# Kernel optimization log

Measured on AMD Instinct MI355X. Metric: run time of the kernel, lower is better.

The kernel has to match this reference:

```python
import jax, jax.numpy as jnp
import numpy as np

L, D, V, BS, H, HD, DL = 12, 768, 50257, 1024, 12, 64, 256
B, T = 2, 1024
EPS = 1e-5


def _ln(x, w, b):
    m = jnp.mean(x, axis=-1, keepdims=True)
    v = jnp.mean((x - m) ** 2, axis=-1, keepdims=True)
    return (x - m) * jax.lax.rsqrt(v + EPS) * w + b


def _rope_tables(t_len):
    inv_freq = 1.0 / (10000.0 ** (jnp.arange(0, HD, 2, dtype=jnp.float32) / HD))
    t = jnp.arange(t_len, dtype=jnp.float32)
    freqs = jnp.outer(t, inv_freq)  # [T, HD/2]
    return jnp.cos(freqs), jnp.sin(freqs)


def _apply_rope(x, cos, sin):
    # x: [B, H, T, HD]; cos/sin: [T, HD/2]
    c = jnp.concatenate([cos, cos], axis=-1)[None, None]
    s = jnp.concatenate([sin, sin], axis=-1)[None, None]
    x1, x2 = jnp.split(x, 2, axis=-1)
    rot = jnp.concatenate([-x2, x1], axis=-1)
    return x * c + rot * s


def setup_inputs() -> dict:
    key = jax.random.key(0)
    ks = jax.random.split(key, 16)
    std = 0.02
    n = lambda k, shape: jax.random.normal(k, shape, dtype=jnp.float32) * std
    return {
        'idx': jax.random.randint(ks[0], (B, T), 0, V),
        'wte': n(ks[1], (V, D)),
        'wpe': n(ks[2], (BS, D)),
        'ln1_w': jnp.ones((L, D)), 'ln1_b': jnp.zeros((L, D)),
        'wq_w': n(ks[3], (L, D, H * HD)), 'wq_b': jnp.zeros((L, H * HD)),
        'kva_w': n(ks[4], (L, D, DL)), 'kva_b': jnp.zeros((L, DL)),
        'kvb_w': n(ks[5], (L, DL, 2 * H * HD)), 'kvb_b': jnp.zeros((L, 2 * H * HD)),
        'out_w': n(ks[6], (L, H * HD, D)), 'out_b': jnp.zeros((L, D)),
        'ln2_w': jnp.ones((L, D)), 'ln2_b': jnp.zeros((L, D)),
        'fc_w': n(ks[7], (L, D, 4 * D)), 'fc_b': jnp.zeros((L, 4 * D)),
        'proj_w': n(ks[8], (L, 4 * D, D)), 'proj_b': jnp.zeros((L, D)),
        'lnf_w': jnp.ones((D,)), 'lnf_b': jnp.zeros((D,)),
    }


def _forward(idx, wte, wpe, ln1_w, ln1_b, wq_w, wq_b, kva_w, kva_b, kvb_w, kvb_b,
             out_w, out_b, ln2_w, ln2_b, fc_w, fc_b, proj_w, proj_b, lnf_w, lnf_b):
    b, t = idx.shape
    x = wte[idx] + wpe[:t][None]  # [B,T,D]
    cos, sin = _rope_tables(t)
    scale = 1.0 / np.sqrt(HD)
    causal = jnp.tril(jnp.ones((t, t), dtype=bool))
    for l in range(L):
        h = _ln(x, ln1_w[l], ln1_b[l])
        q = (h @ wq_w[l] + wq_b[l]).reshape(b, t, H, HD).transpose(0, 2, 1, 3)
        kv_latent = h @ kva_w[l] + kva_b[l]  # [B,T,DL] (the cacheable latent)
        kv = (kv_latent @ kvb_w[l] + kvb_b[l]).reshape(b, t, 2, H, HD)
        kv = kv.transpose(2, 0, 3, 1, 4)  # [2,B,H,T,HD]
        k, v = kv[0], kv[1]
        q = _apply_rope(q, cos, sin)
        k = _apply_rope(k, cos, sin)
        scores = jnp.einsum('bhtd,bhsd->bhts', q, k) * scale
        scores = jnp.where(causal[None, None], scores, -jnp.inf)
        probs = jax.nn.softmax(scores, axis=-1)
        attn = jnp.einsum('bhts,bhsd->bhtd', probs, v)
        attn = attn.transpose(0, 2, 1, 3).reshape(b, t, H * HD)
        x = x + attn @ out_w[l] + out_b[l]
        h2 = _ln(x, ln2_w[l], ln2_b[l])
        mlp = jax.nn.gelu(h2 @ fc_w[l] + fc_b[l], approximate=False) @ proj_w[l] + proj_b[l]
        x = x + mlp
    x = _ln(x, lnf_w, lnf_b)
    logits = x @ wte.T  # tied lm_head
    return logits


def reference(idx, wte, wpe, ln1_w, ln1_b, wq_w, wq_b, kva_w, kva_b, kvb_w, kvb_b,
              out_w, out_b, ln2_w, ln2_b, fc_w, fc_b, proj_w, proj_b, lnf_w, lnf_b):
    return _forward(idx, wte, wpe, ln1_w, ln1_b, wq_w, wq_b, kva_w, kva_b, kvb_w,
                    kvb_b, out_w, out_b, ln2_w, ln2_b, fc_w, fc_b, proj_w, proj_b,
                    lnf_w, lnf_b)
```

## Files before the change

kernel.cpp:

```cpp
#include <hip/hip_runtime.h>
#include <cstdint>
#include <cstddef>


typedef unsigned short ushortT;
typedef __bf16 bf16x8 __attribute__((ext_vector_type(8)));
typedef float f32x4 __attribute__((ext_vector_type(4)));

#define NHEAD 12
#define T_SEQ 1024

__device__ __forceinline__ float bf2f(unsigned short u) {
    union { unsigned int i; float f; } v; v.i = ((unsigned int)u) << 16; return v.f;
}
__device__ __forceinline__ unsigned short f2bf(float f) {
    union { float f; unsigned int i; } v; v.f = f;
    unsigned int r = v.i + 0x7fffu + ((v.i >> 16) & 1u);
    return (unsigned short)(r >> 16);
}
__device__ __forceinline__ unsigned int pack2(float a, float b) {
    return (unsigned int)f2bf(a) | ((unsigned int)f2bf(b) << 16);
}
__device__ __forceinline__ void gload_lds16(const void* g, void* l) {
    __builtin_amdgcn_global_load_lds((__attribute__((address_space(1))) void*)g,
                                     (__attribute__((address_space(3))) void*)l, 16, 0, 0);
}
template <int N>
__device__ __forceinline__ void wait_vmcnt() {
    if constexpr (N == 8)      asm volatile("s_waitcnt vmcnt(8)" ::: "memory");
    else if constexpr (N == 6) asm volatile("s_waitcnt vmcnt(6)" ::: "memory");
    else if constexpr (N == 5) asm volatile("s_waitcnt vmcnt(5)" ::: "memory");
    else if constexpr (N == 4) asm volatile("s_waitcnt vmcnt(4)" ::: "memory");
    else                       asm volatile("s_waitcnt vmcnt(0)" ::: "memory");
}

__global__ __launch_bounds__(256) void transpose_cvt_kernel(
    const float* __restrict__ in, ushortT* __restrict__ outp,
    int K, int N, int outRowOff, size_t outLS) {
    __shared__ float tile[32][33];
    const int tid = threadIdx.x;
    const int n0 = blockIdx.x * 32, k0 = blockIdx.y * 32;
    const float* src = in + (size_t)blockIdx.z * K * N;
    {
        const int r = tid >> 3, cg = tid & 7;
        float4 v = *(const float4*)(src + (size_t)(k0 + r) * N + n0 + cg * 4);
        tile[r][cg * 4 + 0] = v.x; tile[r][cg * 4 + 1] = v.y;
        tile[r][cg * 4 + 2] = v.z; tile[r][cg * 4 + 3] = v.w;
    }
    __syncthreads();
    {
        const int nr = tid >> 3, kg = tid & 7;
        ushort4 o;
        o.x = f2bf(tile[kg * 4 + 0][nr]);
        o.y = f2bf(tile[kg * 4 + 1][nr]);
        o.z = f2bf(tile[kg * 4 + 2][nr]);
        o.w = f2bf(tile[kg * 4 + 3][nr]);
        ushortT* dst = outp + (size_t)blockIdx.z * outLS;
        *(ushort4*)(dst + (size_t)(outRowOff + n0 + nr) * K + k0 + kg * 4) = o;
    }
}

__global__ void cvt_wte_kernel(const float* __restrict__ in, ushortT* __restrict__ outp) {
    size_t i4 = (size_t)blockIdx.x * 256 + threadIdx.x;
    ushort4 o;
    if (i4 < 9649344) {
        float4 v = ((const float4*)in)[i4];
        o.x = f2bf(v.x); o.y = f2bf(v.y); o.z = f2bf(v.z); o.w = f2bf(v.w);
    } else { o.x = 0; o.y = 0; o.z = 0; o.w = 0; }
    ((ushort4*)outp)[i4] = o;
}

__global__ void embed_kernel(const int* __restrict__ idx, const float* __restrict__ wte,
                             const float* __restrict__ wpe, float* __restrict__ x) {
    int i = blockIdx.x * 256 + threadIdx.x;
    int row = i / 768, d = i - row * 768;
    int t = row & 1023;
    x[i] = wte[(size_t)idx[row] * 768 + d] + wpe[(size_t)t * 768 + d];
}

__global__ void rope_tables_kernel(float* __restrict__ cosT, float* __restrict__ sinT) {
    int i = blockIdx.x * 256 + threadIdx.x;
    int t = i >> 5, f = i & 31;
    float invf = exp2f(-(float)f * (13.287712379549449f / 32.0f));
    float ang = (float)t * invf;
    cosT[i] = cosf(ang);
    sinT[i] = sinf(ang);
}

__global__ __launch_bounds__(256) void ln_kernel(const float* __restrict__ x,
                                                 const float* __restrict__ wg,
                                                 const float* __restrict__ bg,
                                                 ushortT* __restrict__ outp) {
    const int row = blockIdx.x, tid = threadIdx.x;
    const float* xr = x + (size_t)row * 768;
    float v0 = xr[tid], v1 = xr[tid + 256], v2 = xr[tid + 512];
    float s = v0 + v1 + v2;
    float ss = v0 * v0 + v1 * v1 + v2 * v2;
#pragma unroll
    for (int off = 32; off >= 1; off >>= 1) {
        s += __shfl_xor(s, off);
        ss += __shfl_xor(ss, off);
    }
    __shared__ float sb[4], ssb[4];
    if ((tid & 63) == 0) { sb[tid >> 6] = s; ssb[tid >> 6] = ss; }
    __syncthreads();
    float S = sb[0] + sb[1] + sb[2] + sb[3];
    float SS = ssb[0] + ssb[1] + ssb[2] + ssb[3];
    const float mean = S * (1.0f / 768.0f);
    float var = SS * (1.0f / 768.0f) - mean * mean;
    const float rs = rsqrtf(var + 1e-5f);
    ushortT* orow = outp + (size_t)row * 768;
    orow[tid]       = f2bf((v0 - mean) * rs * wg[tid]       + bg[tid]);
    orow[tid + 256] = f2bf((v1 - mean) * rs * wg[tid + 256] + bg[tid + 256]);
    orow[tid + 512] = f2bf((v2 - mean) * rs * wg[tid + 512] + bg[tid + 512]);
}

template <int NP>
__global__ __launch_bounds__(256) void reduce_ln_kernel(
    float* __restrict__ x, const float* __restrict__ part,
    const float* __restrict__ bias,
    const float* __restrict__ wg, const float* __restrict__ bg,
    ushortT* __restrict__ outp) {
    const int row = blockIdx.x, tid = threadIdx.x;
    const size_t base = (size_t)row * 768;
    float4 v = {0.f, 0.f, 0.f, 0.f};
    if (tid < 192) {
        v = *(const float4*)(x + base + tid * 4);
        const float4 b4 = *(const float4*)(bias + tid * 4);
        v.x += b4.x; v.y += b4.y; v.z += b4.z; v.w += b4.w;
#pragma unroll
        for (int p = 0; p < NP; ++p) {
            const float4 pv = *(const float4*)(part + (size_t)p * 1572864 + base + tid * 4);
            v.x += pv.x; v.y += pv.y; v.z += pv.z; v.w += pv.w;
        }
        *(float4*)(x + base + tid * 4) = v;
    }
    float s = v.x + v.y + v.z + v.w;
    float ss = v.x * v.x + v.y * v.y + v.z * v.z + v.w * v.w;
#pragma unroll
    for (int off = 32; off >= 1; off >>= 1) {
        s += __shfl_xor(s, off);
        ss += __shfl_xor(ss, off);
    }
    __shared__ float sb[4], ssb[4];
    if ((tid & 63) == 0) { sb[tid >> 6] = s; ssb[tid >> 6] = ss; }
    __syncthreads();
    const float S = sb[0] + sb[1] + sb[2] + sb[3];
    const float SS = ssb[0] + ssb[1] + ssb[2] + ssb[3];
    const float mean = S * (1.0f / 768.0f);
    const float var = SS * (1.0f / 768.0f) - mean * mean;
    const float rs = rsqrtf(var + 1e-5f);
    if (tid < 192) {
        const float4 w4 = *(const float4*)(wg + tid * 4);
        const float4 g4 = *(const float4*)(bg + tid * 4);
        ushort4 o;
        o.x = f2bf((v.x - mean) * rs * w4.x + g4.x);
        o.y = f2bf((v.y - mean) * rs * w4.y + g4.y);
        o.z = f2bf((v.z - mean) * rs * w4.z + g4.z);
        o.w = f2bf((v.w - mean) * rs * w4.w + g4.w);
        *(ushort4*)(outp + base + tid * 4) = o;
    }
}

template <int BM, int NF, int NTHR, bool ROPE, bool PARTIAL = false>
__global__ __launch_bounds__(NTHR) void gemmT(
    const ushortT* __restrict__ A, int lda,
    const ushortT* __restrict__ Bt, int ldb,
    int K, int CS, int Nstore,
    const float* __restrict__ bias0, const float* __restrict__ bias1,
    ushortT* __restrict__ outB0, int ld0,
    ushortT* __restrict__ outB1, int ld1, int mode1,
    const float* __restrict__ resid, float* __restrict__ outF, int ldF,
    int act, const float* __restrict__ cosT, const float* __restrict__ sinT) {
    constexpr int WC = (NTHR == 512) ? 4 : 2;
    constexpr int WMR = BM / 2;
    constexpr int MF = WMR / 16;
    constexpr int NFh = NF / WC;
    constexpr int WNh = NFh * 16;
    constexpr int ABYTES = BM * 128;
    constexpr int BBYTES = NF * 2048;
    constexpr int BUFB = ABYTES + BBYTES;
    constexpr int A_LOADS = (BM * 8) / NTHR;
    constexpr int B_LOADS = (NF * 128) / NTHR;
    constexpr int S = A_LOADS + B_LOADS;
    __shared__ __align__(16) char lds[2 * BUFB];
    const int tid = threadIdx.x;
    const int w = tid >> 6, lane = tid & 63;
    const int wm = w / WC, wn = w % WC;
    const int gx = gridDim.x;
    const int nwg = gx * gridDim.y;
    const int flat = blockIdx.x + gx * blockIdx.y;
    const int xcd = flat & 7, loc = flat >> 3;
    const int qq = nwg >> 3, rr_ = nwg & 7;
    const int swz = (xcd < rr_ ? xcd * (qq + 1) : rr_ * (qq + 1) + (xcd - rr_) * qq) + loc;
    const int m0 = (swz % gx) * BM, n0 = (swz / gx) * NF * 16;
    const int fr = lane & 15, kg = lane >> 4;
    const size_t ldaB = (size_t)lda * 2, ldbB = (size_t)ldb * 2;
    int koff = 0;
    if constexpr (PARTIAL) koff = blockIdx.z * K;
    const char* Ab = (const char*)A + (size_t)koff * 2;
    const char* Bb = (const char*)Bt + (size_t)koff * 2;
    float* outFz = outF;
    if constexpr (PARTIAL) outFz = outF + (size_t)blockIdx.z * 2048 * (size_t)ldF;
    f32x4 acc[MF][NFh] = {};

    auto stage = [&](int buf, int t) {
        const size_t ktB = (size_t)t << 7;
        char* As_ = lds + buf * BUFB;
        char* Bs_ = As_ + ABYTES;
#pragma unroll
        for (int jj = 0; jj < A_LOADS; ++jj) {
            const int i = tid + jj * NTHR;
            const int r = i >> 3, c = i & 7, cc = c ^ (r & 7);
            gload_lds16(Ab + (size_t)(m0 + r) * ldaB + ktB + cc * 16, As_ + i * 16);
        }
#pragma unroll
        for (int jj = 0; jj < B_LOADS; ++jj) {
            const int i = tid + jj * NTHR;
            const int r = i >> 3, c = i & 7, cc = c ^ (r & 7);
            gload_lds16(Bb + (size_t)(n0 + r) * ldbB + ktB + cc * 16, Bs_ + i * 16);
        }
    };

    const int nk = K >> 6;
    stage(0, 0);
    if (nk > 1) { stage(1, 1); wait_vmcnt<S>(); }
    else        { wait_vmcnt<0>(); }
    __builtin_amdgcn_s_barrier();

    for (int t = 0; t < nk; ++t) {
        const int cur = t & 1;
        const char* As_ = lds + cur * BUFB;
        const char* Bs_ = As_ + ABYTES;
        bf16x8 af[MF][2], bfr[NFh][2];
#pragma unroll
        for (int mf = 0; mf < MF; ++mf) {
            const int row = wm * WMR + mf * 16 + fr;
#pragma unroll
            for (int ks = 0; ks < 2; ++ks)
                af[mf][ks] = *(const bf16x8*)(As_ + row * 128 + (((ks * 4 + kg) ^ (row & 7)) << 4));
        }
#pragma unroll
        for (int nf = 0; nf < NFh; ++nf) {
            const int row = wn * WNh + nf * 16 + fr;
#pragma unroll
            for (int ks = 0; ks < 2; ++ks)
                bfr[nf][ks] = *(const bf16x8*)(Bs_ + row * 128 + (((ks * 4 + kg) ^ (row & 7)) << 4));
        }
        if (t + 2 < nk) {
            asm volatile("s_waitcnt lgkmcnt(0)" ::: "memory");
            __builtin_amdgcn_s_barrier();
            stage(cur, t + 2);
        }
#pragma unroll
        for (int ks = 0; ks < 2; ++ks)
#pragma unroll
            for (int nf = 0; nf < NFh; ++nf)
#pragma unroll
                for (int mf = 0; mf < MF; ++mf)
                    acc[mf][nf] = __builtin_amdgcn_mfma_f32_16x16x32_bf16(
                        af[mf][ks], bfr[nf][ks], acc[mf][nf], 0, 0, 0);
        if (t + 1 < nk) {
            if (t + 2 < nk) wait_vmcnt<S>();
            else            wait_vmcnt<0>();
            __builtin_amdgcn_s_barrier();
        }
    }

    if constexpr (ROPE) {
        float vv[MF][4][4];
#pragma unroll
        for (int mf = 0; mf < MF; ++mf)
#pragma unroll
            for (int nf = 0; nf < 4; ++nf) {
                const int gcol = n0 + wn * 64 + nf * 16 + fr;
                float bv = (gcol < CS) ? (bias0 ? bias0[gcol] : 0.0f)
                                       : (bias1 ? bias1[gcol - CS] : 0.0f);
#pragma unroll
                for (int j = 0; j < 4; ++j) vv[mf][nf][j] = acc[mf][nf][j] + bv;
            }
        if (n0 + wn * 64 < 768) {
#pragma unroll
            for (int mf = 0; mf < MF; ++mf)
#pragma unroll
                for (int j = 0; j < 4; ++j) {
                    const int grow = m0 + wm * WMR + mf * 16 + kg * 4 + j;
                    const int t = grow & 1023;
                    const float c0 = cosT[t * 32 + fr],      s0 = sinT[t * 32 + fr];
                    const float c1 = cosT[t * 32 + 16 + fr], s1 = sinT[t * 32 + 16 + fr];
                    float x1 = vv[mf][0][j], x2 = vv[mf][2][j];
                    vv[mf][0][j] = x1 * c0 - x2 * s0;
                    vv[mf][2][j] = x2 * c0 + x1 * s0;
                    float y1 = vv[mf][1][j], y2 = vv[mf][3][j];
                    vv[mf][1][j] = y1 * c1 - y2 * s1;
                    vv[mf][3][j] = y2 * c1 + y1 * s1;
                }
        }
#pragma unroll
        for (int mf = 0; mf < MF; ++mf)
#pragma unroll
            for (int nf = 0; nf < 4; ++nf) {
                const int gcol = n0 + wn * 64 + nf * 16 + fr;
                if (gcol >= Nstore) continue;
#pragma unroll
                for (int j = 0; j < 4; ++j) {
                    const int grow = m0 + wm * WMR + mf * 16 + kg * 4 + j;
                    const float v = vv[mf][nf][j];
                    if (gcol < CS) {
                        if (outB0) outB0[(size_t)grow * ld0 + gcol] = f2bf(v);
                    } else if (outB1) {
                        if (mode1 == 0) {
                            outB1[(size_t)grow * ld1 + gcol - CS] = f2bf(v);
                        } else {
                            const int bb = grow >> 10, tt = grow & 1023;
                            const int hd = gcol - CS;
                            outB1[((size_t)((bb * 12 + (hd >> 6)) * 64 + (hd & 63)) << 10) + tt] = f2bf(v);
                        }
                    }
                }
            }
    } else {
#pragma unroll
        for (int mf = 0; mf < MF; ++mf) {
#pragma unroll
            for (int nf = 0; nf < NFh; ++nf) {
                const int gcol = n0 + wn * WNh + nf * 16 + fr;
                if (gcol >= Nstore) continue;
                float bv = 0.0f;
                if (gcol < CS) { if (bias0) bv = bias0[gcol]; }
                else           { if (bias1) bv = bias1[gcol - CS]; }
#pragma unroll
                for (int j = 0; j < 4; ++j) {
                    const int grow = m0 + wm * WMR + mf * 16 + kg * 4 + j;
                    float v = acc[mf][nf][j] + bv;
                    if (resid) v += resid[(size_t)grow * ldF + gcol];
                    if (act) v = 0.5f * v * (1.0f + erff(v * 0.70710678118654752f));
                    if (outFz) outFz[(size_t)grow * ldF + gcol] = v;
                    if (gcol < CS) {
                        if (outB0) outB0[(size_t)grow * ld0 + gcol] = f2bf(v);
                    } else if (outB1) {
                        if (mode1 == 0) {
                            outB1[(size_t)grow * ld1 + gcol - CS] = f2bf(v);
                        } else {
                            const int bb = grow >> 10, tt = grow & 1023;
                            const int hd = gcol - CS;
                            outB1[((size_t)((bb * 12 + (hd >> 6)) * 64 + (hd & 63)) << 10) + tt] = f2bf(v);
                        }
                    }
                }
            }
        }
    }
}

#define LM_PHASE(SLOT, MB, STAGE_STMT, TAILWAIT)                              \
    {                                                                          \
        bf16x8 af[2][2];                                                       \
        _Pragma("unroll") for (int m = 0; m < 2; ++m)                          \
        _Pragma("unroll") for (int ks = 0; ks < 2; ++ks) {                     \
            const int row = (MB + m) * 16 + fr;                                \
            af[m][ks] = *(const bf16x8*)(Aw + (SLOT) * 32768 + row * 128 +     \
                                         (((ks * 4 + kg) ^ (row & 7)) << 4));  \
        }                                                                      \
        STAGE_STMT;                                                            \
        __builtin_amdgcn_s_barrier();                                          \
        asm volatile("s_waitcnt lgkmcnt(0)" ::: "memory");                     \
        __builtin_amdgcn_sched_barrier(0);                                     \
        __builtin_amdgcn_s_setprio(1);                                         \
        _Pragma("unroll") for (int ks = 0; ks < 2; ++ks)                       \
        _Pragma("unroll") for (int nf = 0; nf < 4; ++nf)                       \
        _Pragma("unroll") for (int m = 0; m < 2; ++m)                          \
            acc[MB + m][nf] = __builtin_amdgcn_mfma_f32_16x16x32_bf16(         \
                af[m][ks], bfr[nf][ks], acc[MB + m][nf], 0, 0, 0);             \
        __builtin_amdgcn_s_setprio(0);                                         \
        TAILWAIT;                                                              \
        __builtin_amdgcn_s_barrier();                                          \
    }

__global__ __launch_bounds__(512, 1) void lmhead8(
    const ushortT* __restrict__ A, const ushortT* __restrict__ Bt,
    float* __restrict__ outF) {
    __shared__ __align__(16) char lds[131072];
    const int tid = threadIdx.x;
    const int w = tid >> 6, lane = tid & 63;
    const int wm = w >> 2, wn = w & 3;
    const int fr = lane & 15, kg = lane >> 4;
    const int flat = blockIdx.x + 8 * blockIdx.y;
    const int swz = (flat & 7) * 197 + (flat >> 3);
    const int m0 = (swz & 7) * 256, n0 = (swz >> 3) * 256;

    const char* Ag = (const char*)A;
    const char* Bg = (const char*)Bt;
    const char* Aw = lds + wm * 16384;
    const char* Bw = lds + 65536 + (wn >> 1) * 16384;
    const int brow0 = (wn & 1) * 64;

    auto stA = [&](int tile, int half) {
        char* dst = lds + (tile & 1) * 32768 + half * 16384;
#pragma unroll
        for (int jj = 0; jj < 2; ++jj) {
            const int i = tid + jj * 512;
            const int r = i >> 3, c = i & 7, cc = c ^ (r & 7);
            gload_lds16(Ag + (size_t)(m0 + half * 128 + r) * 1536 + tile * 128 + cc * 16,
                        dst + i * 16);
        }
    };
    auto stB = [&](int tile, int half) {
        char* dst = lds + 65536 + (tile & 1) * 32768 + half * 16384;
#pragma unroll
        for (int jj = 0; jj < 2; ++jj) {
            const int i = tid + jj * 512;
            const int r = i >> 3, c = i & 7, cc = c ^ (r & 7);
            gload_lds16(Bg + (size_t)(n0 + half * 128 + r) * 1536 + tile * 128 + cc * 16,
                        dst + i * 16);
        }
    };

    f32x4 acc[8][4] = {};
    stA(0, 0); stA(0, 1); stB(0, 0); stB(0, 1); stB(1, 0); stB(1, 1);
    wait_vmcnt<4>();
    __builtin_amdgcn_s_barrier();

    for (int i = 0; i < 6; ++i) {
        const int t1 = 2 * i + 1;
        const bool st = (i < 5);
        bf16x8 bfr[4][2];
#pragma unroll
        for (int nf = 0; nf < 4; ++nf)
#pragma unroll
            for (int ks = 0; ks < 2; ++ks) {
                const int row = brow0 + nf * 16 + fr;
                bfr[nf][ks] = *(const bf16x8*)(Bw + 0 * 32768 + row * 128 +
                                               (((ks * 4 + kg) ^ (row & 7)) << 4));
            }
        LM_PHASE(0, 0, stA(t1, 0), )
        LM_PHASE(0, 2, stA(t1, 1), )
        LM_PHASE(0, 4, if (st) stB(t1 + 1, 0), )
        LM_PHASE(0, 6, if (st) stB(t1 + 1, 1),
                 if (st) { wait_vmcnt<4>(); } else { wait_vmcnt<0>(); }
                 __builtin_amdgcn_sched_barrier(0))
#pragma unroll
        for (int nf = 0; nf < 4; ++nf)
#pragma unroll
            for (int ks = 0; ks < 2; ++ks) {
                const int row = brow0 + nf * 16 + fr;
                bfr[nf][ks] = *(const bf16x8*)(Bw + 1 * 32768 + row * 128 +
                                               (((ks * 4 + kg) ^ (row & 7)) << 4));
            }
        LM_PHASE(1, 0, if (st) stA(t1 + 1, 0), )
        LM_PHASE(1, 2, if (st) stA(t1 + 1, 1), )
        LM_PHASE(1, 4, if (st) stB(t1 + 2, 0), )
        LM_PHASE(1, 6, if (st) stB(t1 + 2, 1),
                 if (st) { wait_vmcnt<4>(); } else { wait_vmcnt<0>(); }
                 __builtin_amdgcn_sched_barrier(0))
    }

#pragma unroll
    for (int mf = 0; mf < 8; ++mf)
#pragma unroll
        for (int nf = 0; nf < 4; ++nf) {
            const int col = n0 + wn * 64 + nf * 16 + fr;
            if (col < 50257) {
#pragma unroll
                for (int j = 0; j < 4; ++j) {
                    const int row = m0 + wm * 128 + mf * 16 + kg * 4 + j;
                    outF[(size_t)row * 50257 + col] = acc[mf][nf][j];
                }
            }
        }
}

__global__ __launch_bounds__(256) void attn_mfma(const ushortT* __restrict__ q,
                                                 const ushortT* __restrict__ kbuf,
                                                 const ushortT* __restrict__ vT,
                                                 ushortT* __restrict__ attnb) {
    __shared__ __align__(16) char lds[41472];
    const int tid = threadIdx.x, w = tid >> 6, lane = tid & 63;
    const int fr = lane & 15, kg = lane >> 4;
    const int flat = blockIdx.x + 16 * blockIdx.y;
    const int nf2 = (flat & 7) * 48 + (flat >> 3);
    const int bh = nf2 >> 4;
    const int b = bh / NHEAD, h = bh % NHEAD;
    const int qb = (15 - (nf2 & 15)) * 64;
    const int q0 = qb + w * 16;
    const int nst = (qb >> 6) + 1, diag = qb >> 6;

    const ushortT* qrow = q + ((size_t)(b * 1024 + q0 + fr) * 768 + h * 64);
    const bf16x8 qf0 = *(const bf16x8*)(qrow + kg * 8);
    const bf16x8 qf1 = *(const bf16x8*)(qrow + 32 + kg * 8);

    const char* kgb = (const char*)kbuf + ((size_t)(b * 1024) * 768 + h * 64) * 2;
    const char* vgb = (const char*)vT + ((size_t)(b * 12 + h) * 65536) * 2;
    char* Pw = lds + 32768 + w * 2176 + fr * 136;

    auto stage = [&](int buf, int st) {
#pragma unroll
        for (int jj = 0; jj < 2; ++jj) {
            const int i = tid + jj * 256;
            const int r = i >> 3, c = i & 7, cc = c ^ (r & 7);
            gload_lds16(kgb + (size_t)(st * 64 + r) * 1536 + cc * 16, lds + buf * 8192 + i * 16);
            gload_lds16(vgb + (size_t)r * 2048 + st * 128 + cc * 16, lds + 16384 + buf * 8192 + i * 16);
        }
    };

    float m_r = -1e30f, l_r = 0.0f;
    f32x4 o[4] = {};

    stage(0, 0);
    if (nst > 1) stage(1, 1);
    for (int st = 0; st < nst; ++st) {
        const int cur = st & 1;
        if (st + 1 < nst) wait_vmcnt<4>();
        else              wait_vmcnt<0>();
        __builtin_amdgcn_s_barrier();
        const char* Kd = lds + cur * 8192;
        const char* Vd = lds + 16384 + cur * 8192;

        f32x4 sfr[4];
        __builtin_amdgcn_s_setprio(1);
#pragma unroll
        for (int n = 0; n < 4; ++n) {
            const int row = n * 16 + fr;
            bf16x8 k0 = *(const bf16x8*)(Kd + row * 128 + ((kg ^ (row & 7)) << 4));
            bf16x8 k1 = *(const bf16x8*)(Kd + row * 128 + (((4 + kg) ^ (row & 7)) << 4));
            f32x4 sa = {0.0f, 0.0f, 0.0f, 0.0f};
            sa = __builtin_amdgcn_mfma_f32_16x16x32_bf16(k0, qf0, sa, 0, 0, 0);
            sa = __builtin_amdgcn_mfma_f32_16x16x32_bf16(k1, qf1, sa, 0, 0, 0);
            sfr[n] = sa;
        }
        __builtin_amdgcn_s_setprio(0);
        const int qoff = w * 16 + fr;
#pragma unroll
        for (int n = 0; n < 4; ++n)
#pragma unroll
            for (int j = 0; j < 4; ++j) {
                float v = sfr[n][j] * 0.125f;
                if (st == diag && (n * 16 + kg * 4 + j) > qoff) v = -1e30f;
                sfr[n][j] = v;
            }
        float tm = -1e30f;
#pragma unroll
        for (int n = 0; n < 4; ++n)
#pragma unroll
            for (int j = 0; j < 4; ++j) tm = fmaxf(tm, sfr[n][j]);
        tm = fmaxf(tm, __shfl_xor(tm, 16));
        tm = fmaxf(tm, __shfl_xor(tm, 32));
        const float mnew = fmaxf(m_r, tm);
        const float fac = __expf(m_r - mnew);
        m_r = mnew;
        l_r *= fac;
        const float ff0 = __shfl(fac, kg * 4 + 0);
        const float ff1 = __shfl(fac, kg * 4 + 1);
        const float ff2 = __shfl(fac, kg * 4 + 2);
        const float ff3 = __shfl(fac, kg * 4 + 3);
#pragma unroll
        for (int nf = 0; nf < 4; ++nf) {
            o[nf][0] *= ff0; o[nf][1] *= ff1; o[nf][2] *= ff2; o[nf][3] *= ff3;
        }
#pragma unroll
        for (int n = 0; n < 4; ++n) {
            float e0 = __expf(sfr[n][0] - mnew);
            float e1 = __expf(sfr[n][1] - mnew);
            float e2 = __expf(sfr[n][2] - mnew);
            float e3 = __expf(sfr[n][3] - mnew);
            l_r += (e0 + e1) + (e2 + e3);
            uint2 pv;
            pv.x = pack2(e0, e1);
            pv.y = pack2(e2, e3);
            *(uint2*)(Pw + n * 32 + kg * 8) = pv;
        }
        __builtin_amdgcn_s_setprio(1);
#pragma unroll
        for (int ks = 0; ks < 2; ++ks) {
            uint2 a0 = *(const uint2*)(Pw + ks * 64 + kg * 16);
            uint2 a1 = *(const uint2*)(Pw + ks * 64 + kg * 16 + 8);
            union { uint4 u; bf16x8 v; } pa;
            pa.u = make_uint4(a0.x, a0.y, a1.x, a1.y);
#pragma unroll
            for (int nf = 0; nf < 4; ++nf) {
                const int row = nf * 16 + fr;
                bf16x8 vf = *(const bf16x8*)(Vd + row * 128 + (((ks * 4 + kg) ^ (row & 7)) << 4));
                o[nf] = __builtin_amdgcn_mfma_f32_16x16x32_bf16(pa.v, vf, o[nf], 0, 0, 0);
            }
        }
        __builtin_amdgcn_s_setprio(0);
        __builtin_amdgcn_s_barrier();
        if (st + 2 < nst) stage(cur, st + 2);
    }

    l_r += __shfl_xor(l_r, 16);
    l_r += __shfl_xor(l_r, 32);
    const float inv = 1.0f / l_r;
    const float iv0 = __shfl(inv, kg * 4 + 0);
    const float iv1 = __shfl(inv, kg * 4 + 1);
    const float iv2 = __shfl(inv, kg * 4 + 2);
    const float iv3 = __shfl(inv, kg * 4 + 3);
#pragma unroll
    for (int nf = 0; nf < 4; ++nf) {
        const size_t base = (size_t)(b * 1024 + q0) * 768 + h * 64 + nf * 16 + fr;
        attnb[base + (size_t)(kg * 4 + 0) * 768] = f2bf(o[nf][0] * iv0);
        attnb[base + (size_t)(kg * 4 + 1) * 768] = f2bf(o[nf][1] * iv1);
        attnb[base + (size_t)(kg * 4 + 2) * 768] = f2bf(o[nf][2] * iv2);
        attnb[base + (size_t)(kg * 4 + 3) * 768] = f2bf(o[nf][3] * iv3);
    }
}

extern "C" void kernel_launch(void* const* d_in, const int* in_sizes, int n_in,
                              void* d_out, int out_size, void* d_ws, size_t ws_size,
                              hipStream_t stream) {
    (void)in_sizes; (void)n_in; (void)out_size; (void)ws_size;
    const int*   idxp   = (const int*)d_in[0];
    const float* wte    = (const float*)d_in[1];
    const float* wpe    = (const float*)d_in[2];
    const float* ln1_w  = (const float*)d_in[3];
    const float* ln1_b  = (const float*)d_in[4];
    const float* wq_w   = (const float*)d_in[5];
    const float* wq_b   = (const float*)d_in[6];
    const float* kva_w  = (const float*)d_in[7];
    const float* kva_b  = (const float*)d_in[8];
    const float* kvb_w  = (const float*)d_in[9];
    const float* kvb_b  = (const float*)d_in[10];
    const float* out_w  = (const float*)d_in[11];
    const float* out_b  = (const float*)d_in[12];
    const float* ln2_w  = (const float*)d_in[13];
    const float* ln2_b  = (const float*)d_in[14];
    const float* fc_w   = (const float*)d_in[15];
    const float* fc_b   = (const float*)d_in[16];
    const float* proj_w = (const float*)d_in[17];
    const float* proj_b = (const float*)d_in[18];
    const float* lnf_w  = (const float*)d_in[19];
    const float* lnf_b  = (const float*)d_in[20];

    char* ws = (char*)d_ws;
    size_t off = 0;
    auto alloc = [&](size_t bytes) -> char* {
        char* p = ws + off;
        off += (bytes + 255) & ~(size_t)255;
        return p;
    };
    ushortT* wqkvaT = (ushortT*)alloc((size_t)12 * 1024 * 768 * 2);
    ushortT* kvbT   = (ushortT*)alloc((size_t)12 * 1536 * 256 * 2);
    ushortT* outT   = (ushortT*)alloc((size_t)12 * 768 * 768 * 2);
    ushortT* fcT    = (ushortT*)alloc((size_t)12 * 3072 * 768 * 2);
    ushortT* projT  = (ushortT*)alloc((size_t)12 * 768 * 3072 * 2);
    ushortT* wteB   = (ushortT*)alloc((size_t)50432 * 768 * 2);
    float* cosT = (float*)alloc((size_t)1024 * 32 * 4);
    float* sinT = (float*)alloc((size_t)1024 * 32 * 4);
    float*   x     = (float*)alloc((size_t)2048 * 768 * 4);
    ushortT* h     = (ushortT*)alloc((size_t)2048 * 768 * 2);
    ushortT* qbuf  = (ushortT*)alloc((size_t)2048 * 768 * 2);
    ushortT* lat   = (ushortT*)alloc((size_t)2048 * 256 * 2);
    ushortT* kvbuf = (ushortT*)alloc((size_t)2048 * 768 * 2);
    ushortT* vTb   = (ushortT*)alloc((size_t)24 * 64 * 1024 * 2);
    ushortT* attnb = (ushortT*)alloc((size_t)2048 * 768 * 2);
    ushortT* fca   = (ushortT*)alloc((size_t)2048 * 3072 * 2);
    float*   partB = (float*)alloc((size_t)4 * 2048 * 768 * 4);

    transpose_cvt_kernel<<<dim3(24, 24, 12), 256, 0, stream>>>(wq_w,  wqkvaT, 768, 768,  0,   (size_t)1024 * 768);
    transpose_cvt_kernel<<<dim3(8,  24, 12), 256, 0, stream>>>(kva_w, wqkvaT, 768, 256,  768, (size_t)1024 * 768);
    transpose_cvt_kernel<<<dim3(48, 8,  12), 256, 0, stream>>>(kvb_w, kvbT,   256, 1536, 0,   (size_t)1536 * 256);
    transpose_cvt_kernel<<<dim3(24, 24, 12), 256, 0, stream>>>(out_w, outT,   768, 768,  0,   (size_t)768 * 768);
    transpose_cvt_kernel<<<dim3(96, 24, 12), 256, 0, stream>>>(fc_w,  fcT,    768, 3072, 0,   (size_t)3072 * 768);
    transpose_cvt_kernel<<<dim3(24, 96, 12), 256, 0, stream>>>(proj_w, projT, 3072, 768, 0,   (size_t)768 * 3072);
    cvt_wte_kernel<<<37824, 256, 0, stream>>>(wte, wteB);
    rope_tables_kernel<<<128, 256, 0, stream>>>(cosT, sinT);
    embed_kernel<<<6144, 256, 0, stream>>>(idxp, wte, wpe, x);
    ln_kernel<<<2048, 256, 0, stream>>>(x, ln1_w, ln1_b, h);

    for (int l = 0; l < 12; ++l) {
        gemmT<64, 8, 256, true><<<dim3(32, 8), 256, 0, stream>>>(
            h, 768, wqkvaT + (size_t)l * 1024 * 768, 768,
            768, 768, 1024, wq_b + l * 768, kva_b + l * 256,
            qbuf, 768, lat, 256, 0, nullptr, nullptr, 0, 0, cosT, sinT);
        gemmT<64, 8, 256, true><<<dim3(32, 12), 256, 0, stream>>>(
            lat, 256, kvbT + (size_t)l * 1536 * 256, 256,
            256, 768, 1536, kvb_b + l * 1536, kvb_b + l * 1536 + 768,
            kvbuf, 768, vTb, 0, 1, nullptr, nullptr, 0, 0, cosT, sinT);
        attn_mfma<<<dim3(16, 24), 256, 0, stream>>>(qbuf, kvbuf, vTb, attnb);
        gemmT<64, 8, 256, false, true><<<dim3(32, 6, 2), 256, 0, stream>>>(
            attnb, 768, outT + (size_t)l * 768 * 768, 768,
            384, 768, 768, nullptr, nullptr,
            nullptr, 0, nullptr, 0, 0, nullptr, partB, 768, 0, nullptr, nullptr);
        reduce_ln_kernel<2><<<2048, 256, 0, stream>>>(
            x, partB, out_b + l * 768, ln2_w + l * 768, ln2_b + l * 768, h);
        gemmT<128, 12, 512, false><<<dim3(16, 16), 512, 0, stream>>>(
            h, 768, fcT + (size_t)l * 3072 * 768, 768,
            768, 3072, 3072, fc_b + l * 3072, nullptr,
            fca, 3072, nullptr, 0, 0, nullptr, nullptr, 0, 1, nullptr, nullptr);
        gemmT<64, 8, 256, false, true><<<dim3(32, 6, 4), 256, 0, stream>>>(
            fca, 3072, projT + (size_t)l * 768 * 3072, 3072,
            768, 768, 768, nullptr, nullptr,
            nullptr, 0, nullptr, 0, 0, nullptr, partB, 768, 0, nullptr, nullptr);
        const float* nw = (l < 11) ? ln1_w + (l + 1) * 768 : lnf_w;
        const float* nb = (l < 11) ? ln1_b + (l + 1) * 768 : lnf_b;
        reduce_ln_kernel<4><<<2048, 256, 0, stream>>>(
            x, partB, proj_b + l * 768, nw, nb, h);
    }
    lmhead8<<<dim3(8, 197), 512, 0, stream>>>(h, wteB, (float*)d_out);
}
```

Baseline: 1.898 ms.

## Add 8-wave 128x256 pipelined GEMM kernel for MLP fc and proj layers

Adds a dedicated gemm8 kernel with 8 waves and 128x256 output tiles. It double-buffers A and B in LDS with swizzled layout, interleaves async global-to-LDS loads with MFMA phases, and remaps workgroups in an XCD-aware order. The kernel replaces the generic gemmT for the MLP up-projection (fused bias+GELU) and for the split-K down-projection. The goal is better latency hiding and data reuse in the two largest per-layer GEMMs. The trade-offs are fewer workgroups per launch, and a kernel that hardcodes K=768 per split and 768-wide partial outputs.

```diff
diff --git a/kernel.cpp b/kernel.cpp
--- a/kernel.cpp
+++ b/kernel.cpp
@@ -353,6 +353,132 @@
     }
 }
 
+#define FC_PHASE(SLOT, MB, STAGE_STMT, TAILWAIT)                               \
+    {                                                                          \
+        bf16x8 af[2][2];                                                       \
+        _Pragma("unroll") for (int m = 0; m < 2; ++m)                          \
+        _Pragma("unroll") for (int ks = 0; ks < 2; ++ks) {                     \
+            const int row = wm * 64 + (MB + m) * 16 + fr;                      \
+            af[m][ks] = *(const bf16x8*)(lds + (SLOT) * 16384 + row * 128 +    \
+                                         (((ks * 4 + kg) ^ (row & 7)) << 4));  \
+        }                                                                      \
+        STAGE_STMT;                                                            \
+        __builtin_amdgcn_s_barrier();                                          \
+        asm volatile("s_waitcnt lgkmcnt(0)" ::: "memory");                     \
+        __builtin_amdgcn_sched_barrier(0);                                     \
+        __builtin_amdgcn_s_setprio(1);                                         \
+        _Pragma("unroll") for (int ks = 0; ks < 2; ++ks)                       \
+        _Pragma("unroll") for (int nf = 0; nf < 4; ++nf)                       \
+        _Pragma("unroll") for (int m = 0; m < 2; ++m)                          \
+            acc[MB + m][nf] = __builtin_amdgcn_mfma_f32_16x16x32_bf16(         \
+                af[m][ks], bfr[nf][ks], acc[MB + m][nf], 0, 0, 0);             \
+        __builtin_amdgcn_s_setprio(0);                                         \
+        TAILWAIT;                                                              \
+        __builtin_amdgcn_s_barrier();                                          \
+    }
+
+template <bool GELU, bool PARTIAL>
+__global__ __launch_bounds__(512, 1) void gemm8(
+    const ushortT* __restrict__ A, int lda,
+    const ushortT* __restrict__ Bt, int ldb,
+    const float* __restrict__ bias,
+    ushortT* __restrict__ outB, int ldo,
+    float* __restrict__ outF) {
+    __shared__ __align__(16) char lds[98304];
+    const int tid = threadIdx.x;
+    const int w = tid >> 6, lane = tid & 63;
+    const int wm = w >> 2, wn = w & 3;
+    const int fr = lane & 15, kg = lane >> 4;
+    const int gx = gridDim.x;
+    const int nwg = gx * gridDim.y;
+    const int flat = blockIdx.x + gx * blockIdx.y;
+    const int cpx = nwg >> 3;
+    const int swz = (flat & 7) * cpx + (flat >> 3);
+    const int m0 = (swz % gx) * 128, n0 = (swz / gx) * 256;
+    const size_t ldaB = (size_t)lda * 2, ldbB = (size_t)ldb * 2;
+    int koff = 0;
+    if constexpr (PARTIAL) koff = blockIdx.z * 768;
+    const char* Ag = (const char*)A + (size_t)koff * 2;
+    const char* Bg = (const char*)Bt + (size_t)koff * 2;
+    float* outFz = nullptr;
+    if constexpr (PARTIAL) outFz = outF + (size_t)blockIdx.z * 2048 * 768;
+
+    auto stA = [&](int tile) {
+        char* dst = lds + (tile & 1) * 16384;
+#pragma unroll
+        for (int jj = 0; jj < 2; ++jj) {
+            const int i = tid + jj * 512;
+            const int r = i >> 3, c = i & 7, cc = c ^ (r & 7);
+            gload_lds16(Ag + (size_t)(m0 + r) * ldaB + tile * 128 + cc * 16, dst + i * 16);
+        }
+    };
+    auto stB = [&](int tile, int half) {
+        char* dst = lds + 32768 + (tile & 1) * 32768 + half * 16384;
+#pragma unroll
+        for (int jj = 0; jj < 2; ++jj) {
+            const int i = tid + jj * 512;
+            const int r = i >> 3, c = i & 7, cc = c ^ (r & 7);
+            gload_lds16(Bg + (size_t)(n0 + half * 128 + r) * ldbB + tile * 128 + cc * 16,
+                        dst + i * 16);
+        }
+    };
+
+    f32x4 acc[4][4] = {};
+    stA(0); stB(0, 0); stB(0, 1); stB(1, 0); stB(1, 1);
+    wait_vmcnt<4>();
+    __builtin_amdgcn_s_barrier();
+
+    const int browB = wn * 64;
+    for (int i = 0; i < 6; ++i) {
+        const int t1 = 2 * i + 1;
+        const bool st = (i < 5);
+        bf16x8 bfr[4][2];
+#pragma unroll
+        for (int nf = 0; nf < 4; ++nf)
+#pragma unroll
+            for (int ks = 0; ks < 2; ++ks) {
+                const int row = browB + nf * 16 + fr;
+                bfr[nf][ks] = *(const bf16x8*)(lds + 32768 + 0 * 32768 + row * 128 +
+                                               (((ks * 4 + kg) ^ (row & 7)) << 4));
+            }
+        FC_PHASE(0, 0, stA(t1), )
+        FC_PHASE(0, 2, if (st) { stB(t1 + 1, 0); stB(t1 + 1, 1); },
+                 if (st) { wait_vmcnt<4>(); } else { wait_vmcnt<0>(); }
+                 __builtin_amdgcn_sched_barrier(0))
+#pragma unroll
+        for (int nf = 0; nf < 4; ++nf)
+#pragma unroll
+            for (int ks = 0; ks < 2; ++ks) {
+                const int row = browB + nf * 16 + fr;
+                bfr[nf][ks] = *(const bf16x8*)(lds + 32768 + 1 * 32768 + row * 128 +
+                                               (((ks * 4 + kg) ^ (row & 7)) << 4));
+            }
+        FC_PHASE(1, 0, if (st) stA(t1 + 1), )
+        FC_PHASE(1, 2, if (st) { stB(t1 + 2, 0); stB(t1 + 2, 1); },
+                 if (st) { wait_vmcnt<4>(); } else { wait_vmcnt<0>(); }
+                 __builtin_amdgcn_sched_barrier(0))
+    }
+
+#pragma unroll
+    for (int mf = 0; mf < 4; ++mf)
+#pragma unroll
+        for (int nf = 0; nf < 4; ++nf) {
+            const int col = n0 + wn * 64 + nf * 16 + fr;
+#pragma unroll
+            for (int j = 0; j < 4; ++j) {
+                const int row = m0 + wm * 64 + mf * 16 + kg * 4 + j;
+                if constexpr (PARTIAL) {
+                    outFz[(size_t)row * 768 + col] = acc[mf][nf][j];
+                } else {
+                    float v = acc[mf][nf][j] + bias[col];
+                    if constexpr (GELU)
+                        v = 0.5f * v * (1.0f + erff(v * 0.70710678118654752f));
+                    outB[(size_t)row * ldo + col] = f2bf(v);
+                }
+            }
+        }
+}
+
 #define LM_PHASE(SLOT, MB, STAGE_STMT, TAILWAIT)                              \
     {                                                                          \
         bf16x8 af[2][2];                                                       \
@@ -683,14 +809,12 @@
             nullptr, 0, nullptr, 0, 0, nullptr, partB, 768, 0, nullptr, nullptr);
         reduce_ln_kernel<2><<<2048, 256, 0, stream>>>(
             x, partB, out_b + l * 768, ln2_w + l * 768, ln2_b + l * 768, h);
-        gemmT<128, 12, 512, false><<<dim3(16, 16), 512, 0, stream>>>(
+        gemm8<true, false><<<dim3(16, 12), 512, 0, stream>>>(
             h, 768, fcT + (size_t)l * 3072 * 768, 768,
-            768, 3072, 3072, fc_b + l * 3072, nullptr,
-            fca, 3072, nullptr, 0, 0, nullptr, nullptr, 0, 1, nullptr, nullptr);
-        gemmT<64, 8, 256, false, true><<<dim3(32, 6, 4), 256, 0, stream>>>(
+            fc_b + l * 3072, fca, 3072, nullptr);
+        gemm8<false, true><<<dim3(16, 3, 4), 512, 0, stream>>>(
             fca, 3072, projT + (size_t)l * 768 * 3072, 3072,
-            768, 768, 768, nullptr, nullptr,
-            nullptr, 0, nullptr, 0, 0, nullptr, partB, 768, 0, nullptr, nullptr);
+            nullptr, nullptr, 0, partB);
         const float* nw = (l < 11) ? ln1_w + (l + 1) * 768 : lnf_w;
         const float* nb = (l < 11) ? ln1_b + (l + 1) * 768 : lnf_b;
         reduce_ln_kernel<4><<<2048, 256, 0, stream>>>(
```

Result: faster. 1.819 ms (-4.1%).
